# Kernel tuning notes

Hardware: AMD Instinct MI355X
Metric: run time of the kernel (lower is better)

## Reference

```python
import jax, jax.numpy as jnp
import numpy as np
from functools import partial


def advect(f, vx, vy):
    """Semi-Lagrangian advection with bilinear interpolation and periodic wrap.
    Faithful to the torch version, including its xy-indexed meshgrid."""
    rows, cols = f.shape
    # torch.meshgrid(arange(rows), arange(cols), indexing='xy') == np.meshgrid semantics
    cell_ys, cell_xs = jnp.meshgrid(jnp.arange(rows), jnp.arange(cols), indexing='xy')
    center_xs = (cell_xs - vx).ravel()
    center_ys = (cell_ys - vy).ravel()
    left_ix = jnp.floor(center_xs).astype(jnp.int32)
    top_ix = jnp.floor(center_ys).astype(jnp.int32)
    rw = center_xs - left_ix  # right weight
    bw = center_ys - top_ix   # bottom weight
    left_ix = jnp.mod(left_ix, rows)
    right_ix = jnp.mod(left_ix + 1, rows)
    top_ix = jnp.mod(top_ix, cols)
    bot_ix = jnp.mod(top_ix + 1, cols)
    flat_f = ((1 - rw) * ((1 - bw) * f[left_ix, top_ix] + bw * f[left_ix, bot_ix])
              + rw * ((1 - bw) * f[right_ix, top_ix] + bw * f[right_ix, bot_ix]))
    return flat_f.reshape(rows, cols)


def project(vx, vy):
    """Approximate pressure projection: 10 Jacobi iterations of a 5-point stencil."""
    h = 1.0 / vx.shape[0]
    div = -0.5 * h * (jnp.roll(vx, -1, axis=0) - jnp.roll(vx, 1, axis=0)
                      + jnp.roll(vy, -1, axis=1) - jnp.roll(vy, 1, axis=1))

    def jacobi(k, p):
        return (div + jnp.roll(p, 1, axis=0) + jnp.roll(p, -1, axis=0)
                + jnp.roll(p, 1, axis=1) + jnp.roll(p, -1, axis=1)) / 4.0

    p = jax.lax.fori_loop(0, 10, jacobi, jnp.zeros_like(vx))
    vx = vx - 0.5 * (jnp.roll(p, -1, axis=0) - jnp.roll(p, 1, axis=0)) / h
    vy = vy - 0.5 * (jnp.roll(p, -1, axis=1) - jnp.roll(p, 1, axis=1)) / h
    return vx, vy


def simulate(vx, vy, smoke, num_time_steps):
    def step(carry, _):
        vx, vy, smoke = carry
        vx_upd = advect(vx, vx, vy)
        vy_upd = advect(vy, vx, vy)
        vx, vy = project(vx_upd, vy_upd)
        smoke = advect(smoke, vx, vy)
        return (vx, vy, smoke), None

    (vx, vy, smoke), _ = jax.lax.scan(step, (vx, vy, smoke), None, length=num_time_steps)
    return smoke


def setup_inputs() -> dict:
    key = jax.random.key(0)
    k1, k2, k3 = jax.random.split(key, 3)
    N = 2048
    smoke = jax.random.uniform(k1, (N, N), dtype=jnp.float32)
    init_vx = jax.random.normal(k2, (N, N), dtype=jnp.float32)
    init_vy = jax.random.normal(k3, (N, N), dtype=jnp.float32)
    return {"smoke": smoke, "init_vx": init_vx, "init_vy": init_vy,
            "num_time_steps": 20}


def reference(smoke, init_vx, init_vy, num_time_steps):
    return simulate(init_vx, init_vy, smoke, num_time_steps)
```

## Files before the change

kernel.cpp:

```cpp
#include <hip/hip_runtime.h>

namespace {

constexpr int N = 2048;
constexpr int MASK = N - 1;
constexpr int SH = 11;
constexpr float H = 1.0f / (float)N;

constexpr int LSTR = 64;
constexpr int ROWS = 54;

__device__ __forceinline__ float dpp_left(float x) {
  return __int_as_float(__builtin_amdgcn_update_dpp(
      0, __float_as_int(x), 0x111 , 0xF, 0xF, true));
}
__device__ __forceinline__ float dpp_right(float x) {
  return __int_as_float(__builtin_amdgcn_update_dpp(
      0, __float_as_int(x), 0x101 , 0xF, 0xF, true));
}

__global__ __launch_bounds__(256) void advect_vel_k(
    const float* __restrict__ vx, const float* __restrict__ vy,
    float* __restrict__ ovx, float* __restrict__ ovy) {
  int bid = blockIdx.x;
  int sb = ((bid & 7) << 11) | (bid >> 3);
  int idx = sb * 256 + threadIdx.x;
  int i = idx >> SH, j = idx & MASK;
  float cx = (float)i - vx[idx];
  float cy = (float)j - vy[idx];
  float fx = floorf(cx), fy = floorf(cy);
  float rw = cx - fx, bw = cy - fy;
  int l = ((int)fx) & MASK;
  int t = ((int)fy) & MASK;
  int r = (l + 1) & MASK;
  int b = (t + 1) & MASK;
  int i00 = (l << SH) | t, i01 = (l << SH) | b;
  int i10 = (r << SH) | t, i11 = (r << SH) | b;
  float omr = 1.0f - rw, omb = 1.0f - bw;
  float w00 = omr * omb, w01 = omr * bw, w10 = rw * omb, w11 = rw * bw;
  ovx[idx] = w00 * vx[i00] + w01 * vx[i01] + w10 * vx[i10] + w11 * vx[i11];
  ovy[idx] = w00 * vy[i00] + w01 * vy[i01] + w10 * vy[i10] + w11 * vy[i11];
}

__global__ __launch_bounds__(512, 8) void project_smoke_k(
    const float* __restrict__ vx, const float* __restrict__ vy,
    const float* __restrict__ f,
    float* __restrict__ ovx, float* __restrict__ ovy,
    float* __restrict__ of) {
  __shared__ __align__(16) float pA[ROWS * LSTR];
  __shared__ __align__(16) float pB[ROWS * LSTR];

  const int tid = threadIdx.x;
  const int bid = blockIdx.x;
  const int sbid = ((bid & 7) << 9) | (bid >> 3);
  const int tile_i = sbid >> 6;
  const int tile_j = sbid & 63;
  const int bi = tile_i * 32 - 11;
  const int cj0 = tile_j * 32 - 16;

  for (int e = tid; e < ROWS * 16; e += 512) {
    int qq = e & 15;
    int ii = e >> 4;
    int gi = (bi + ii) & MASK;
    int gj = (cj0 + qq * 4) & MASK;
    int g = (gi << SH) | gj;
    float4 x4 = *(const float4*)&vx[g];
    float4 y4 = *(const float4*)&vy[g];
    *(float4*)&pA[ii * LSTR + qq * 4] = x4;
    *(float4*)&pB[ii * LSTR + qq * 4] = y4;
  }
  __syncthreads();

  float vxc[2], vyc[2];
#pragma unroll
  for (int q = 0; q < 2; ++q) {
    int pth = tid + q * 512;
    int oi = pth >> 5, oj = pth & 31;
    vxc[q] = pA[(11 + oi) * LSTR + 16 + oj];
    vyc[q] = pB[(11 + oi) * LSTR + 16 + oj];
  }

  const int qc4 = (tid & 15) * 4;
  const int r0 = tid >> 4;
  float4 p[2], d[2];
#pragma unroll
  for (int q = 0; q < 2; ++q) { p[q] = float4{0,0,0,0}; d[q] = float4{0,0,0,0}; }

#pragma unroll
  for (int q = 0; q < 2; ++q) {
    int row = r0 + 32 * q;
    if (row >= 1 && row <= 52) {
      float4 xu = *(const float4*)&pA[(row - 1) * LSTR + qc4];
      float4 xd = *(const float4*)&pA[(row + 1) * LSTR + qc4];
      float4 yc = *(const float4*)&pB[row * LSTR + qc4];
      float yl = dpp_left(yc.w);
      float yr = dpp_right(yc.x);
      constexpr float s = -0.5f * H;
      d[q].x = s * ((xd.x - xu.x) + (yc.y - yl));
      d[q].y = s * ((xd.y - xu.y) + (yc.z - yc.x));
      d[q].z = s * ((xd.z - xu.z) + (yc.w - yc.y));
      d[q].w = s * ((xd.w - xu.w) + (yr - yc.z));
      p[q].x = d[q].x * 0.25f;
      p[q].y = d[q].y * 0.25f;
      p[q].z = d[q].z * 0.25f;
      p[q].w = d[q].w * 0.25f;
    }
  }
  __syncthreads();

#pragma unroll
  for (int k = 0; k < 9; ++k) {
    float* w = (k & 1) ? pB : pA;
#pragma unroll
    for (int q = 0; q < 2; ++q) {
      int row = r0 + 32 * q;
      if (row >= k + 1 && row <= 52 - k)
        *(float4*)&w[row * LSTR + qc4] = p[q];
    }
    __syncthreads();
#pragma unroll
    for (int q = 0; q < 2; ++q) {
      int row = r0 + 32 * q;
      if (row >= k + 2 && row <= 51 - k) {
        float4 up = *(const float4*)&w[(row - 1) * LSTR + qc4];
        float4 dn = *(const float4*)&w[(row + 1) * LSTR + qc4];
        float pl = dpp_left(p[q].w);
        float pr = dpp_right(p[q].x);
        float4 np;
        np.x = (d[q].x + up.x + dn.x + pl     + p[q].y) * 0.25f;
        np.y = (d[q].y + up.y + dn.y + p[q].x + p[q].z) * 0.25f;
        np.z = (d[q].z + up.z + dn.z + p[q].y + p[q].w) * 0.25f;
        np.w = (d[q].w + up.w + dn.w + p[q].z + pr    ) * 0.25f;
        p[q] = np;
      }
    }
  }

#pragma unroll
  for (int q = 0; q < 2; ++q) {
    int row = r0 + 32 * q;
    if (row >= 10 && row <= 43)
      *(float4*)&pB[row * LSTR + qc4] = p[q];
  }
  __syncthreads();

  const float c = 0.5f / H;
#pragma unroll
  for (int q = 0; q < 2; ++q) {
    int pth = tid + q * 512;
    int oi = pth >> 5, oj = pth & 31;
    int ii = 11 + oi, jj = 16 + oj;
    float nvx = vxc[q] - c * (pB[(ii + 1) * LSTR + jj] - pB[(ii - 1) * LSTR + jj]);
    float nvy = vyc[q] - c * (pB[ii * LSTR + jj + 1]   - pB[ii * LSTR + jj - 1]);
    int gi = tile_i * 32 + oi;
    int gj = tile_j * 32 + oj;
    int g = (gi << SH) | gj;
    ovx[g] = nvx;
    ovy[g] = nvy;
    float cx = (float)gi - nvx;
    float cy = (float)gj - nvy;
    float fx = floorf(cx), fy = floorf(cy);
    float rw = cx - fx, bw = cy - fy;
    int l = ((int)fx) & MASK;
    int t = ((int)fy) & MASK;
    int r = (l + 1) & MASK;
    int b = (t + 1) & MASK;
    float f00 = f[(l << SH) | t];
    float f01 = f[(l << SH) | b];
    float f10 = f[(r << SH) | t];
    float f11 = f[(r << SH) | b];
    float omr = 1.0f - rw, omb = 1.0f - bw;
    of[g] = omr * (omb * f00 + bw * f01) + rw * (omb * f10 + bw * f11);
  }
}

}

extern "C" void kernel_launch(void* const* d_in, const int* in_sizes, int n_in,
                              void* d_out, int out_size, void* d_ws, size_t ws_size,
                              hipStream_t stream) {
  const float* smoke_in = (const float*)d_in[0];
  const float* vx_in    = (const float*)d_in[1];
  const float* vy_in    = (const float*)d_in[2];
  float* out = (float*)d_out;

  const size_t fsz = (size_t)N * N;
  float* base = (float*)d_ws;
  float* A  = base + 0 * fsz;
  float* B  = base + 1 * fsz;
  float* C  = base + 2 * fsz;
  float* D  = base + 3 * fsz;
  float* SA = base + 4 * fsz;

  dim3 ablk(256), agrd((N * N) / 256);
  dim3 pblk(512), pgrd(64 * 64);
  const int steps = 20;

  const float* ssrc = smoke_in;

  advect_vel_k<<<agrd, ablk, 0, stream>>>(vx_in, vy_in, C, D);

  for (int t = 0; t < steps; ++t) {
    float* sdst = (t & 1) ? out : SA;
    project_smoke_k<<<pgrd, pblk, 0, stream>>>(C, D, ssrc, A, B, sdst);
    ssrc = sdst;
    if (t < steps - 1)
      advect_vel_k<<<agrd, ablk, 0, stream>>>(A, B, C, D);
  }
}
```

Before: 1.190 ms.

## Register-block Jacobi rows per thread and exchange only edge rows via LDS

The project kernel moves from 512 threads to 256 threads per block. Each active thread now holds four consecutive rows of pressure in registers, loads velocity straight from global memory instead of staging tiles in LDS, and writes only its first and last rows to a compact shared halo buffer on each Jacobi iteration. The goal is to cut LDS traffic and footprint and raise occupancy, since interior vertical neighbours come from registers. In exchange, 32 of the 256 threads sit idle, register pressure rises, and the center velocities are read again from global memory.

```diff
diff --git a/kernel.cpp b/kernel.cpp
--- a/kernel.cpp
+++ b/kernel.cpp
@@ -7,8 +7,6 @@
 constexpr int SH = 11;
 constexpr float H = 1.0f / (float)N;
 
-constexpr int LSTR = 64;
-constexpr int ROWS = 54;
 
 __device__ __forceinline__ float dpp_left(float x) {
   return __int_as_float(__builtin_amdgcn_update_dpp(
@@ -42,13 +40,12 @@
   ovy[idx] = w00 * vy[i00] + w01 * vy[i01] + w10 * vy[i10] + w11 * vy[i11];
 }
 
-__global__ __launch_bounds__(512, 8) void project_smoke_k(
+__global__ __launch_bounds__(256, 8) void project_smoke_k(
     const float* __restrict__ vx, const float* __restrict__ vy,
     const float* __restrict__ f,
     float* __restrict__ ovx, float* __restrict__ ovy,
     float* __restrict__ of) {
-  __shared__ __align__(16) float pA[ROWS * LSTR];
-  __shared__ __align__(16) float pB[ROWS * LSTR];
+  __shared__ __align__(16) float lds[3584];
 
   const int tid = threadIdx.x;
   const int bid = blockIdx.x;
@@ -58,107 +55,111 @@
   const int bi = tile_i * 32 - 11;
   const int cj0 = tile_j * 32 - 16;
 
-  for (int e = tid; e < ROWS * 16; e += 512) {
-    int qq = e & 15;
-    int ii = e >> 4;
-    int gi = (bi + ii) & MASK;
-    int gj = (cj0 + qq * 4) & MASK;
-    int g = (gi << SH) | gj;
-    float4 x4 = *(const float4*)&vx[g];
-    float4 y4 = *(const float4*)&vy[g];
-    *(float4*)&pA[ii * LSTR + qq * 4] = x4;
-    *(float4*)&pB[ii * LSTR + qq * 4] = y4;
-  }
+  const int s = tid >> 4;
+  const int qc4 = (tid & 15) * 4;
+  const bool act = (s < 14);
+  const int gj = (cj0 + qc4) & MASK;
+
+  float4 p[4], d[4];
+#pragma unroll
+  for (int m = 0; m < 4; ++m) {
+    p[m] = float4{0.f, 0.f, 0.f, 0.f};
+    d[m] = float4{0.f, 0.f, 0.f, 0.f};
+  }
+
+  if (act) {
+    const int r0g = bi + 4 * s;
+    float4 vxr[6], vyr[4];
+#pragma unroll
+    for (int m = 0; m < 6; ++m)
+      vxr[m] = *(const float4*)&vx[(((r0g - 1 + m) & MASK) << SH) | gj];
+#pragma unroll
+    for (int m = 0; m < 4; ++m)
+      vyr[m] = *(const float4*)&vy[(((r0g + m) & MASK) << SH) | gj];
+#pragma unroll
+    for (int m = 0; m < 4; ++m) {
+      int row = 4 * s + m;
+      float yl = dpp_left(vyr[m].w);
+      float yr = dpp_right(vyr[m].x);
+      if (row >= 1 && row <= 52) {
+        constexpr float sc = -0.5f * H;
+        d[m].x = sc * ((vxr[m + 2].x - vxr[m].x) + (vyr[m].y - yl));
+        d[m].y = sc * ((vxr[m + 2].y - vxr[m].y) + (vyr[m].z - vyr[m].x));
+        d[m].z = sc * ((vxr[m + 2].z - vxr[m].z) + (vyr[m].w - vyr[m].y));
+        d[m].w = sc * ((vxr[m + 2].w - vxr[m].w) + (yr - vyr[m].z));
+        p[m].x = d[m].x * 0.25f;
+        p[m].y = d[m].y * 0.25f;
+        p[m].z = d[m].z * 0.25f;
+        p[m].w = d[m].w * 0.25f;
+      }
+    }
+  }
+
+  const int upslot = (s == 0) ? 0 : 2 * s - 1;
+  const int dnslot = (s >= 13) ? 27 : 2 * s + 2;
+
+#pragma unroll
+  for (int k = 0; k < 9; ++k) {
+    float* w = &lds[(k & 1) * 1792];
+    if (act) {
+      if (4 * s >= k + 1 && 4 * s <= 52 - k)
+        *(float4*)&w[(2 * s) * 64 + qc4] = p[0];
+      if (4 * s + 3 >= k + 1 && 4 * s + 3 <= 52 - k)
+        *(float4*)&w[(2 * s + 1) * 64 + qc4] = p[3];
+    }
+    __syncthreads();
+    if (act) {
+      float4 up = *(const float4*)&w[upslot * 64 + qc4];
+      float4 dn = *(const float4*)&w[dnslot * 64 + qc4];
+      float4 tprev;
+#pragma unroll
+      for (int m = 0; m < 4; ++m) {
+        float4 vu = (m == 0) ? up : tprev;
+        float4 vd = (m == 3) ? dn : p[m + 1];
+        float pl = dpp_left(p[m].w);
+        float pr = dpp_right(p[m].x);
+        float4 old = p[m];
+        int row = 4 * s + m;
+        if (row >= k + 2 && row <= 51 - k) {
+          float4 np;
+          np.x = (d[m].x + vu.x + vd.x + pl    + old.y) * 0.25f;
+          np.y = (d[m].y + vu.y + vd.y + old.x + old.z) * 0.25f;
+          np.z = (d[m].z + vu.z + vd.z + old.y + old.w) * 0.25f;
+          np.w = (d[m].w + vu.w + vd.w + old.z + pr   ) * 0.25f;
+          p[m] = np;
+        }
+        tprev = old;
+      }
+    }
+  }
+
   __syncthreads();
-
-  float vxc[2], vyc[2];
-#pragma unroll
-  for (int q = 0; q < 2; ++q) {
-    int pth = tid + q * 512;
+  if (act) {
+#pragma unroll
+    for (int m = 0; m < 4; ++m) {
+      int row = 4 * s + m;
+      if (row >= 10 && row <= 43)
+        *(float4*)&lds[(row - 10) * 64 + qc4] = p[m];
+    }
+  }
+  __syncthreads();
+
+  const float c = 0.5f / H;
+#pragma unroll
+  for (int qq = 0; qq < 4; ++qq) {
+    int pth = tid + qq * 256;
     int oi = pth >> 5, oj = pth & 31;
-    vxc[q] = pA[(11 + oi) * LSTR + 16 + oj];
-    vyc[q] = pB[(11 + oi) * LSTR + 16 + oj];
-  }
-
-  const int qc4 = (tid & 15) * 4;
-  const int r0 = tid >> 4;
-  float4 p[2], d[2];
-#pragma unroll
-  for (int q = 0; q < 2; ++q) { p[q] = float4{0,0,0,0}; d[q] = float4{0,0,0,0}; }
-
-#pragma unroll
-  for (int q = 0; q < 2; ++q) {
-    int row = r0 + 32 * q;
-    if (row >= 1 && row <= 52) {
-      float4 xu = *(const float4*)&pA[(row - 1) * LSTR + qc4];
-      float4 xd = *(const float4*)&pA[(row + 1) * LSTR + qc4];
-      float4 yc = *(const float4*)&pB[row * LSTR + qc4];
-      float yl = dpp_left(yc.w);
-      float yr = dpp_right(yc.x);
-      constexpr float s = -0.5f * H;
-      d[q].x = s * ((xd.x - xu.x) + (yc.y - yl));
-      d[q].y = s * ((xd.y - xu.y) + (yc.z - yc.x));
-      d[q].z = s * ((xd.z - xu.z) + (yc.w - yc.y));
-      d[q].w = s * ((xd.w - xu.w) + (yr - yc.z));
-      p[q].x = d[q].x * 0.25f;
-      p[q].y = d[q].y * 0.25f;
-      p[q].z = d[q].z * 0.25f;
-      p[q].w = d[q].w * 0.25f;
-    }
-  }
-  __syncthreads();
-
-#pragma unroll
-  for (int k = 0; k < 9; ++k) {
-    float* w = (k & 1) ? pB : pA;
-#pragma unroll
-    for (int q = 0; q < 2; ++q) {
-      int row = r0 + 32 * q;
-      if (row >= k + 1 && row <= 52 - k)
-        *(float4*)&w[row * LSTR + qc4] = p[q];
-    }
-    __syncthreads();
-#pragma unroll
-    for (int q = 0; q < 2; ++q) {
-      int row = r0 + 32 * q;
-      if (row >= k + 2 && row <= 51 - k) {
-        float4 up = *(const float4*)&w[(row - 1) * LSTR + qc4];
-        float4 dn = *(const float4*)&w[(row + 1) * LSTR + qc4];
-        float pl = dpp_left(p[q].w);
-        float pr = dpp_right(p[q].x);
-        float4 np;
-        np.x = (d[q].x + up.x + dn.x + pl     + p[q].y) * 0.25f;
-        np.y = (d[q].y + up.y + dn.y + p[q].x + p[q].z) * 0.25f;
-        np.z = (d[q].z + up.z + dn.z + p[q].y + p[q].w) * 0.25f;
-        np.w = (d[q].w + up.w + dn.w + p[q].z + pr    ) * 0.25f;
-        p[q] = np;
-      }
-    }
-  }
-
-#pragma unroll
-  for (int q = 0; q < 2; ++q) {
-    int row = r0 + 32 * q;
-    if (row >= 10 && row <= 43)
-      *(float4*)&pB[row * LSTR + qc4] = p[q];
-  }
-  __syncthreads();
-
-  const float c = 0.5f / H;
-#pragma unroll
-  for (int q = 0; q < 2; ++q) {
-    int pth = tid + q * 512;
-    int oi = pth >> 5, oj = pth & 31;
-    int ii = 11 + oi, jj = 16 + oj;
-    float nvx = vxc[q] - c * (pB[(ii + 1) * LSTR + jj] - pB[(ii - 1) * LSTR + jj]);
-    float nvy = vyc[q] - c * (pB[ii * LSTR + jj + 1]   - pB[ii * LSTR + jj - 1]);
     int gi = tile_i * 32 + oi;
-    int gj = tile_j * 32 + oj;
-    int g = (gi << SH) | gj;
+    int gjc = tile_j * 32 + oj;
+    int g = (gi << SH) | gjc;
+    float vxc = vx[g];
+    float vyc = vy[g];
+    float nvx = vxc - c * (lds[(oi + 2) * 64 + 16 + oj] - lds[(oi + 0) * 64 + 16 + oj]);
+    float nvy = vyc - c * (lds[(oi + 1) * 64 + 17 + oj] - lds[(oi + 1) * 64 + 15 + oj]);
     ovx[g] = nvx;
     ovy[g] = nvy;
     float cx = (float)gi - nvx;
-    float cy = (float)gj - nvy;
+    float cy = (float)gjc - nvy;
     float fx = floorf(cx), fy = floorf(cy);
     float rw = cx - fx, bw = cy - fy;
     int l = ((int)fx) & MASK;
@@ -193,7 +194,7 @@
   float* SA = base + 4 * fsz;
 
   dim3 ablk(256), agrd((N * N) / 256);
-  dim3 pblk(512), pgrd(64 * 64);
+  dim3 pblk(256), pgrd(64 * 64);
   const int steps = 20;
 
   const float* ssrc = smoke_in;
```

New measurement: 1.273 ms. 1.07x slower.
